# Performance work log

Measured on AMD Instinct MI355X. Metric: run time of the kernel, lower is better.

## Reference

```python
import jax, jax.numpy as jnp
import numpy as np

GRID_N = 8
N_RAYS = 4096
CHUNK = 512
MAX_SAMPLES = 128
SAMPLING_LENGTH = 0.05
STEP = SAMPLING_LENGTH / MAX_SAMPLES
HIT_THRESH = 5.0


def _build_mesh(n):
    g = n + 1
    xs = np.linspace(0.0, 1.0, g)
    P = np.stack(np.meshgrid(xs, xs, xs, indexing='ij'), -1).reshape(-1, 3).astype(np.float32)

    def vid(i, j, k):
        return (i * g + j) * g + k

    perms = [(0, 1, 2), (0, 2, 1), (1, 0, 2), (1, 2, 0), (2, 0, 1), (2, 1, 0)]
    tets = []
    for i in range(n):
        for j in range(n):
            for k in range(n):
                base = np.array([i, j, k])
                for p in perms:
                    vlist = [base.copy()]
                    cur = base.copy()
                    for ax in p:
                        cur = cur.copy(); cur[ax] += 1
                        vlist.append(cur.copy())
                    tets.append([vid(*vv) for vv in vlist])
    tets = np.array(tets, dtype=np.int32)  # [T,4]
    A, B, C, D = tets.T
    # face order matches torch module: ABC, ABD, ACD, BCD
    faces = np.stack([np.stack([A, B, C], 1), np.stack([A, B, D], 1),
                      np.stack([A, C, D], 1), np.stack([B, C, D], 1)], 1).astype(np.int32)  # [T,4,3]
    ff = faces.reshape(-1, 3)
    sf = np.sort(ff, 1)
    order = np.lexsort((sf[:, 2], sf[:, 1], sf[:, 0]))
    ss = sf[order]
    eq = np.all(ss[:-1] == ss[1:], 1)
    topo = -np.ones((tets.shape[0], 4), dtype=np.int32)
    idx = np.where(eq)[0]
    a = order[idx]; b = order[idx + 1]
    topo[a // 4, a % 4] = b // 4
    topo[b // 4, b % 4] = a // 4
    return P, tets, faces, topo


def setup_inputs() -> dict:
    key = jax.random.key(0)
    k1, k2, k3 = jax.random.split(key, 3)
    P, tets, faces, topo = _build_mesh(GRID_N)
    cage = jnp.asarray(P)[None] + 0.005 * jax.random.normal(k1, (1, P.shape[0], 3), jnp.float32)
    xy = jax.random.uniform(k2, (N_RAYS, 2), jnp.float32, 0.15, 0.85)
    ro = jnp.concatenate([xy, jnp.full((N_RAYS, 1), -0.5, jnp.float32)], -1)[None]
    jit = 0.05 * jax.random.normal(k3, (N_RAYS, 2), jnp.float32)
    rd = jnp.concatenate([jit, jnp.ones((N_RAYS, 1), jnp.float32)], -1)
    rd = (rd / jnp.linalg.norm(rd, axis=-1, keepdims=True))[None]
    return {"cage_vertices": cage, "ro": ro, "rd": rd,
            "tetras": jnp.asarray(tets), "faces": jnp.asarray(faces),
            "topology": jnp.asarray(topo)}


def _intersect(tri, o, d):
    # Moller-Trumbore: tri [F,3,3], o/d [c,3] -> nearest hit t + face idx
    p0 = tri[:, 0]; e1 = tri[:, 1] - p0; e2 = tri[:, 2] - p0
    h = jnp.cross(d[:, None, :], e2[None])          # [c,F,3]
    a = jnp.sum(e1[None] * h, -1)                   # [c,F]
    f = 1.0 / jnp.where(jnp.abs(a) > 1e-9, a, 1e-9)
    s = o[:, None, :] - p0[None]
    u = f * jnp.sum(s * h, -1)
    q = jnp.cross(s, e1[None])
    v = f * jnp.sum(d[:, None, :] * q, -1)
    t = f * jnp.sum(e2[None] * q, -1)
    ok = (jnp.abs(a) > 1e-9) & (u >= 0) & (u <= 1) & (v >= 0) & (u + v <= 1) & (t > 1e-6)
    t = jnp.where(ok, t, 1e10)
    return jnp.min(t, 1), jnp.argmin(t, 1)


def _bary(verts, tetras, p, tet):
    # barycentric coords of p [R,3] inside tetra tet [R] -> [R,4]
    vv = verts[tetras[tet]]                                # [R,4,3]
    M = jnp.transpose(vv[:, 1:] - vv[:, :1], (0, 2, 1))    # [R,3,3] columns B-A,C-A,D-A
    w = jnp.linalg.solve(M, (p - vv[:, 0])[..., None])[..., 0]  # wB,wC,wD
    return jnp.concatenate([1.0 - jnp.sum(w, -1, keepdims=True), w], -1)


def reference(cage_vertices, ro, rd, tetras, faces, topology):
    verts = cage_vertices[0]                 # [V,3]
    tri = verts[faces.reshape(-1, 3)]        # [F,3,3] deformed tetra faces
    o = ro[0]; d = rd[0]
    R = o.shape[0]
    od = jnp.concatenate([o, d], -1).reshape(R // CHUNK, CHUNK, 6)
    tmin, fidx = jax.lax.map(lambda x: _intersect(tri, x[:, :3], x[:, 3:]), od)
    tmin = tmin.reshape(R); fidx = fidx.reshape(R)
    hit = tmin < HIT_THRESH                  # mask = distances < 5
    t0 = jnp.where(hit, tmin, 0.0)
    hitp = o + t0[:, None] * d               # closest_points
    tet0 = jnp.where(hit, (fidx // 4).astype(jnp.int32), 0)  # triangle_to_tetra

    def step(carry, k):
        tet, alive = carry
        p = hitp + (k.astype(jnp.float32) * STEP + 1e-4) * d
        for _ in range(3):  # up to 3 neighbor hops per sample (tetra walk)
            w = _bary(verts, tetras, p, tet)
            inside = jnp.all(w >= -1e-6, -1)
            nb = topology[tet, 3 - jnp.argmin(w, -1)]  # face opposite most-negative vert
            move = alive & ~inside
            tet = jnp.where(move & (nb >= 0), nb, tet)
            alive = alive & (inside | (nb >= 0))
        w = _bary(verts, tetras, p, tet)
        inside = jnp.all(w >= -1e-6, -1)
        valid = alive & inside
        m = valid[:, None].astype(w.dtype)
        return (tet, alive), (jnp.where(valid, tet, -1), w * m, p * m, valid)

    (_, _), (tet_s, w_s, p_s, valid_s) = jax.lax.scan(step, (tet0, hit), jnp.arange(MAX_SAMPLES))
    tetra_indices = jnp.transpose(tet_s)            # [R,S]
    bary_coords = jnp.transpose(w_s, (1, 0, 2))     # [R,S,4]
    deformed_positions = jnp.transpose(p_s, (1, 0, 2))  # [R,S,3]
    valid = jnp.transpose(valid_s)
    ray_indices = jnp.where(valid, jnp.arange(R, dtype=jnp.int32)[:, None], -1)
    t_start = t0
    t_end = jnp.where(hit, t0 + SAMPLING_LENGTH, 0.0)
    return ray_indices, tetra_indices, bary_coords, t_start, t_end, deformed_positions
```

## Files before the change

### kernel.cpp

```cpp
#include <hip/hip_runtime.h>

#define S_MAX 128
#define NV_MAX 729
#define STEPD (0.05 / 128.0)
#define GUARD 1e-12

static __device__ __forceinline__ double mt_eval_f64(
    int F, const int* __restrict__ faces,
    const float* sx, const float* sy, const float* sz,
    double ox, double oy, double oz,
    double dx, double dy, double dz)
{
    const int i0 = faces[3 * F + 0];
    const int i1 = faces[3 * F + 1];
    const int i2 = faces[3 * F + 2];
    const double p0x = (double)sx[i0], p0y = (double)sy[i0], p0z = (double)sz[i0];
    const double e1x = (double)sx[i1] - p0x, e1y = (double)sy[i1] - p0y, e1z = (double)sz[i1] - p0z;
    const double e2x = (double)sx[i2] - p0x, e2y = (double)sy[i2] - p0y, e2z = (double)sz[i2] - p0z;
    const double hx = dy * e2z - dz * e2y;
    const double hy = dz * e2x - dx * e2z;
    const double hz = dx * e2y - dy * e2x;
    const double a  = e1x * hx + e1y * hy + e1z * hz;
    const bool oka = fabs(a) > 1e-9;
    const double f  = 1.0 / (oka ? a : 1e-9);
    const double s0 = ox - p0x, s1 = oy - p0y, s2 = oz - p0z;
    const double u  = f * (s0 * hx + s1 * hy + s2 * hz);
    const double qx = s1 * e1z - s2 * e1y;
    const double qy = s2 * e1x - s0 * e1z;
    const double qz = s0 * e1y - s1 * e1x;
    const double v  = f * (dx * qx + dy * qy + dz * qz);
    double t        = f * (e2x * qx + e2y * qy + e2z * qz);
    const bool ok = oka && (u >= 0.0) && (u <= 1.0) && (v >= 0.0) &&
                    (u + v <= 1.0) && (t > 1e-6);
    return ok ? t : 1e10;
}

__global__ __launch_bounds__(256) void prep_kernel(
    const float* __restrict__ verts,
    const int*   __restrict__ tetras,
    double* __restrict__ winv,
    int NT)
{
    const int t = blockIdx.x * 256 + threadIdx.x;
    if (t >= NT) return;
    const int4 tv = ((const int4*)tetras)[t];
    const double v0x = (double)verts[3 * tv.x + 0];
    const double v0y = (double)verts[3 * tv.x + 1];
    const double v0z = (double)verts[3 * tv.x + 2];
    const double m11 = (double)verts[3 * tv.y + 0] - v0x, m21 = (double)verts[3 * tv.y + 1] - v0y, m31 = (double)verts[3 * tv.y + 2] - v0z;
    const double m12 = (double)verts[3 * tv.z + 0] - v0x, m22 = (double)verts[3 * tv.z + 1] - v0y, m32 = (double)verts[3 * tv.z + 2] - v0z;
    const double m13 = (double)verts[3 * tv.w + 0] - v0x, m23 = (double)verts[3 * tv.w + 1] - v0y, m33 = (double)verts[3 * tv.w + 2] - v0z;
    const double A = m22 * m33 - m23 * m32;
    const double B = m21 * m33 - m23 * m31;
    const double C = m21 * m32 - m22 * m31;
    const double det = m11 * A - m12 * B + m13 * C;
    const double rcp = 1.0 / det;
    double* o = winv + 12 * (size_t)t;
    o[0] = v0x; o[1] = v0y; o[2] = v0z;
    o[3]  = A * rcp;  o[4]  = (m13 * m32 - m12 * m33) * rcp;  o[5]  = (m12 * m23 - m13 * m22) * rcp;
    o[6]  = -B * rcp; o[7]  = (m11 * m33 - m13 * m31) * rcp;  o[8]  = (m13 * m21 - m11 * m23) * rcp;
    o[9]  = C * rcp;  o[10] = (m12 * m31 - m11 * m32) * rcp;  o[11] = (m11 * m22 - m12 * m21) * rcp;
}

__global__ __launch_bounds__(256) void fused_kernel(
    const float* __restrict__ verts,
    const float* __restrict__ ro,
    const float* __restrict__ rd,
    const int*   __restrict__ faces,
    const int*   __restrict__ topo,
    const double* __restrict__ winv,
    float* __restrict__ out_rayidx,
    float* __restrict__ out_tetidx,
    float* __restrict__ out_bary,
    float* __restrict__ out_tstart,
    float* __restrict__ out_tend,
    float* __restrict__ out_pos,
    int NV, int NF, int R)
{
    __shared__ float sx[NV_MAX], sy[NV_MAX], sz[NV_MAX];
    __shared__ float red[256];
    __shared__ float s_zmin, s_zmax, s_marg;
    __shared__ short s_seq[4][S_MAX];

    const int tid = threadIdx.x;
    for (int i = tid; i < NV; i += 256) {
        sx[i] = verts[3 * i + 0];
        sy[i] = verts[3 * i + 1];
        sz[i] = verts[3 * i + 2];
    }
    __syncthreads();

    float zmin = 1e9f, zmax = -1e9f, dev = 0.0f;
    for (int i = tid; i < NV; i += 256) {
        const float x = sx[i], y = sy[i], z = sz[i];
        if (i % 9 == 0) { zmin = fminf(zmin, z); zmax = fmaxf(zmax, z); }
        dev = fmaxf(dev, fabsf(x - rintf(x * 8.0f) * 0.125f));
        dev = fmaxf(dev, fabsf(y - rintf(y * 8.0f) * 0.125f));
    }
    red[tid] = zmin; __syncthreads();
    for (int s = 128; s; s >>= 1) { if (tid < s) red[tid] = fminf(red[tid], red[tid + s]); __syncthreads(); }
    if (tid == 0) s_zmin = red[0];
    __syncthreads();
    red[tid] = zmax; __syncthreads();
    for (int s = 128; s; s >>= 1) { if (tid < s) red[tid] = fmaxf(red[tid], red[tid + s]); __syncthreads(); }
    if (tid == 0) s_zmax = red[0];
    __syncthreads();
    red[tid] = dev; __syncthreads();
    for (int s = 128; s; s >>= 1) { if (tid < s) red[tid] = fmaxf(red[tid], red[tid + s]); __syncthreads(); }
    if (tid == 0) s_marg = red[0] + 1e-5f;
    __syncthreads();

    const int wv = tid >> 6, lane = tid & 63;
    const int r = blockIdx.x * 4 + wv;
    if (r >= R) return;
    short* myseq = s_seq[wv];

    const double ox = (double)ro[3 * r + 0], oy = (double)ro[3 * r + 1], oz = (double)ro[3 * r + 2];
    const double dx = (double)rd[3 * r + 0], dy = (double)rd[3 * r + 1], dz = (double)rd[3 * r + 2];

    int ncand = 0, ixlo = 0, iylo = 0, ny = 1;
    if (dz > 0.0) {
        const double t_lo = ((double)s_zmin - oz) / dz;
        const double t_hi = ((double)s_zmax - oz) / dz;
        const double marg = (double)s_marg + 1e-9;
        const double xa = ox + t_lo * dx, xb = ox + t_hi * dx;
        const double ya = oy + t_lo * dy, yb = oy + t_hi * dy;
        const double xlo = fmin(xa, xb) - marg, xhi = fmax(xa, xb) + marg;
        const double ylo = fmin(ya, yb) - marg, yhi = fmax(ya, yb) + marg;
        const int ix0 = max(0, (int)floor(xlo * 8.0)), ix1 = min(7, (int)floor(xhi * 8.0));
        const int iy0 = max(0, (int)floor(ylo * 8.0)), iy1 = min(7, (int)floor(yhi * 8.0));
        if (ix0 <= ix1 && iy0 <= iy1) {
            ixlo = ix0; iylo = iy0;
            ny = iy1 - iy0 + 1;
            ncand = (ix1 - ix0 + 1) * ny * 24;
        }
    }

    double bt = 1e10;
    int    bi = 0x7fffffff;
    for (int c = lane; c < ncand; c += 64) {
        const int cell = c / 24, fk = c - cell * 24;
        const int cx = cell / ny, cy = cell - cx * ny;
        const int F = ((ixlo + cx) * 64 + (iylo + cy) * 8) * 24 + fk;
        const double t = mt_eval_f64(F, faces, sx, sy, sz, ox, oy, oz, dx, dy, dz);
        if (t < bt || (t == bt && F < bi)) { bt = t; bi = F; }
    }
    for (int off = 32; off; off >>= 1) {
        const double t2 = __shfl_down(bt, off);
        const int    i2 = __shfl_down(bi, off);
        if (t2 < bt || (t2 == bt && i2 < bi)) { bt = t2; bi = i2; }
    }
    bt = __shfl(bt, 0);
    bi = __shfl(bi, 0);
    if (bt >= 1e10) {
        double fb = 1e10; int fi = 0x7fffffff;
        for (int F = lane; F < NF; F += 64) {
            const double t = mt_eval_f64(F, faces, sx, sy, sz, ox, oy, oz, dx, dy, dz);
            if (t < fb || (t == fb && F < fi)) { fb = t; fi = F; }
        }
        for (int off = 32; off; off >>= 1) {
            const double t2 = __shfl_down(fb, off);
            const int    i2 = __shfl_down(fi, off);
            if (t2 < fb || (t2 == fb && i2 < fi)) { fb = t2; fi = i2; }
        }
        bt = __shfl(fb, 0);
        bi = __shfl(fi, 0);
    }

    const bool   hit = bt < 5.0;
    const double t0  = hit ? bt : 0.0;
    if (lane == 0) {
        out_tstart[r] = (float)t0;
        out_tend[r]   = hit ? (float)(t0 + 0.05) : 0.0f;
    }

    const double hpx = ox + t0 * dx, hpy = oy + t0 * dy, hpz = oz + t0 * dz;

    if (!hit) {
        for (int k = lane; k < S_MAX; k += 64) myseq[k] = -1;
    } else {
        int  tet   = bi >> 2;
        bool alive = true;

        int4 topo4 = ((const int4*)topo)[tet];
        const double* rec = winv + 12 * (size_t)tet;
        double v0x = rec[0], v0y = rec[1], v0z = rec[2];
        double i0 = rec[3], i1 = rec[4],  i2 = rec[5];
        double i3 = rec[6], i4 = rec[7],  i5 = rec[8];
        double i6 = rec[9], i7 = rec[10], i8 = rec[11];

        double wb0, wb1, wb2, wb3, wd0, wd1, wd2, wd3;
        {
            const double bx = hpx - v0x, by = hpy - v0y, bz = hpz - v0z;
            wb1 = i0 * bx + i1 * by + i2 * bz;
            wb2 = i3 * bx + i4 * by + i5 * bz;
            wb3 = i6 * bx + i7 * by + i8 * bz;
            wd1 = i0 * dx + i1 * dy + i2 * dz;
            wd2 = i3 * dx + i4 * dy + i5 * dz;
            wd3 = i6 * dx + i7 * dy + i8 * dz;
            wb0 = 1.0 - (wb1 + wb2 + wb3);
            wd0 = -(wd1 + wd2 + wd3);
        }

        int k0 = 0;
        while (k0 < S_MAX) {
            const int kk = k0 + lane;
            bool p = false;
            if (kk < S_MAX) {
                const double toff = (double)kk * STEPD + 1e-4;
                const double a0 = wb0 + toff * wd0;
                const double a1 = wb1 + toff * wd1;
                const double a2 = wb2 + toff * wd2;
                const double a3 = wb3 + toff * wd3;
                const double mn = fmin(fmin(a0, a1), fmin(a2, a3));
                p = (mn + 1e-6 >= GUARD);
            }
            const unsigned long long bad = __ballot(kk < S_MAX && !p);
            const int nvalid = min(S_MAX - k0, 64);
            const int evt = (bad == 0ull) ? nvalid : (__ffsll(bad) - 1);

            if (lane < evt) myseq[kk] = (short)tet;
            k0 += evt;
            if (evt == nvalid) continue;

            const double toff = (double)k0 * STEPD + 1e-4;
            const double px = hpx + toff * dx;
            const double py = hpy + toff * dy;
            const double pz = hpz + toff * dz;

            double b1 = px - v0x, b2 = py - v0y, b3 = pz - v0z;
            double w1 = i0 * b1 + i1 * b2 + i2 * b3;
            double w2 = i3 * b1 + i4 * b2 + i5 * b3;
            double w3 = i6 * b1 + i7 * b2 + i8 * b3;
            double w0 = 1.0 - (w1 + w2 + w3);
            bool inside = (w0 >= -1e-6) && (w1 >= -1e-6) && (w2 >= -1e-6) && (w3 >= -1e-6);

            int it = 0;
            bool moved = false;
            while (!inside && it < 3) {
                int    jm = 0;
                double wb = w0;
                if (w1 < wb) { wb = w1; jm = 1; }
                if (w2 < wb) { wb = w2; jm = 2; }
                if (w3 < wb) { wb = w3; jm = 3; }
                const int nb = (jm == 0) ? topo4.w : (jm == 1) ? topo4.z :
                               (jm == 2) ? topo4.y : topo4.x;
                if (nb < 0) { alive = false; break; }
                tet = nb;
                moved = true;
                rec = winv + 12 * (size_t)tet;
                topo4 = ((const int4*)topo)[tet];
                v0x = rec[0]; v0y = rec[1]; v0z = rec[2];
                i0 = rec[3]; i1 = rec[4];  i2 = rec[5];
                i3 = rec[6]; i4 = rec[7];  i5 = rec[8];
                i6 = rec[9]; i7 = rec[10]; i8 = rec[11];
                b1 = px - v0x; b2 = py - v0y; b3 = pz - v0z;
                w1 = i0 * b1 + i1 * b2 + i2 * b3;
                w2 = i3 * b1 + i4 * b2 + i5 * b3;
                w3 = i6 * b1 + i7 * b2 + i8 * b3;
                w0 = 1.0 - (w1 + w2 + w3);
                inside = (w0 >= -1e-6) && (w1 >= -1e-6) && (w2 >= -1e-6) && (w3 >= -1e-6);
                ++it;
            }
            if (!alive) break;

            if (lane == 0) myseq[k0] = inside ? (short)tet : (short)-1;
            ++k0;

            if (moved) {
                const double bx = hpx - v0x, by = hpy - v0y, bz = hpz - v0z;
                wb1 = i0 * bx + i1 * by + i2 * bz;
                wb2 = i3 * bx + i4 * by + i5 * bz;
                wb3 = i6 * bx + i7 * by + i8 * bz;
                wd1 = i0 * dx + i1 * dy + i2 * dz;
                wd2 = i3 * dx + i4 * dy + i5 * dz;
                wd3 = i6 * dx + i7 * dy + i8 * dz;
                wb0 = 1.0 - (wb1 + wb2 + wb3);
                wd0 = -(wd1 + wd2 + wd3);
            }
        }
        for (int k = k0 + lane; k < S_MAX; k += 64) myseq[k] = -1;
    }

    for (int k = lane; k < S_MAX; k += 64) {
        const size_t idx = (size_t)r * S_MAX + k;
        const int tk = (int)myseq[k];
        if (tk < 0) {
            out_rayidx[idx] = -1.0f;
            out_tetidx[idx] = -1.0f;
            ((float4*)out_bary)[idx] = make_float4(0.0f, 0.0f, 0.0f, 0.0f);
            out_pos[idx * 3 + 0] = 0.0f;
            out_pos[idx * 3 + 1] = 0.0f;
            out_pos[idx * 3 + 2] = 0.0f;
            continue;
        }
        const double toff = (double)k * STEPD + 1e-4;
        const double px = hpx + toff * dx;
        const double py = hpy + toff * dy;
        const double pz = hpz + toff * dz;

        const double* rec2 = winv + 12 * (size_t)tk;
        const double b1 = px - rec2[0], b2 = py - rec2[1], b3 = pz - rec2[2];
        const double w1 = rec2[3] * b1 + rec2[4]  * b2 + rec2[5]  * b3;
        const double w2 = rec2[6] * b1 + rec2[7]  * b2 + rec2[8]  * b3;
        const double w3 = rec2[9] * b1 + rec2[10] * b2 + rec2[11] * b3;
        const double w0 = 1.0 - (w1 + w2 + w3);

        out_rayidx[idx] = (float)r;
        out_tetidx[idx] = (float)tk;
        ((float4*)out_bary)[idx] = make_float4((float)w0, (float)w1, (float)w2, (float)w3);
        out_pos[idx * 3 + 0] = (float)px;
        out_pos[idx * 3 + 1] = (float)py;
        out_pos[idx * 3 + 2] = (float)pz;
    }
}

extern "C" void kernel_launch(void* const* d_in, const int* in_sizes, int n_in,
                              void* d_out, int out_size, void* d_ws, size_t ws_size,
                              hipStream_t stream) {
    const float* verts  = (const float*)d_in[0];
    const float* ro     = (const float*)d_in[1];
    const float* rd     = (const float*)d_in[2];
    const int*   tetras = (const int*)d_in[3];
    const int*   faces  = (const int*)d_in[4];
    const int*   topo   = (const int*)d_in[5];

    const int NV = in_sizes[0] / 3;
    const int R  = in_sizes[1] / 3;
    const int NT = in_sizes[3] / 4;
    const int NF = in_sizes[4] / 3;
    const int S  = S_MAX;

    double* winv = (double*)d_ws;

    float* out        = (float*)d_out;
    float* out_rayidx = out;
    float* out_tetidx = out + (size_t)R * S;
    float* out_bary   = out + (size_t)2 * R * S;
    float* out_tstart = out + (size_t)6 * R * S;
    float* out_tend   = out_tstart + R;
    float* out_pos    = out_tend + R;

    prep_kernel<<<(NT + 255) / 256, 256, 0, stream>>>(verts, tetras, winv, NT);
    fused_kernel<<<(R + 3) / 4, 256, 0, stream>>>(
        verts, ro, rd, faces, topo, winv,
        out_rayidx, out_tetidx, out_bary, out_tstart, out_tend, out_pos,
        NV, NF, R);
}
```

Measured before the change: 83.40 us.

## Drop prep kernel, compute tetra inverses on the fly, write outputs directly

Removes the separate prep kernel that precomputed per-tetra inverse matrices into workspace. Each ray now rebuilds the inverse from vertices already held in shared memory whenever it enters a new tetra. It also drops the shared-memory sequence buffer and writes outputs straight from the walk loop instead of in a second pass that reloaded the inverse records. This saves one launch and a global-memory round trip, at the cost of repeated fp64 inverse computation (including a divide) on each tetra change.

```diff
diff --git a/kernel.cpp b/kernel.cpp
--- a/kernel.cpp
+++ b/kernel.cpp
@@ -35,40 +35,13 @@
     return ok ? t : 1e10;
 }
 
-__global__ __launch_bounds__(256) void prep_kernel(
-    const float* __restrict__ verts,
-    const int*   __restrict__ tetras,
-    double* __restrict__ winv,
-    int NT)
-{
-    const int t = blockIdx.x * 256 + threadIdx.x;
-    if (t >= NT) return;
-    const int4 tv = ((const int4*)tetras)[t];
-    const double v0x = (double)verts[3 * tv.x + 0];
-    const double v0y = (double)verts[3 * tv.x + 1];
-    const double v0z = (double)verts[3 * tv.x + 2];
-    const double m11 = (double)verts[3 * tv.y + 0] - v0x, m21 = (double)verts[3 * tv.y + 1] - v0y, m31 = (double)verts[3 * tv.y + 2] - v0z;
-    const double m12 = (double)verts[3 * tv.z + 0] - v0x, m22 = (double)verts[3 * tv.z + 1] - v0y, m32 = (double)verts[3 * tv.z + 2] - v0z;
-    const double m13 = (double)verts[3 * tv.w + 0] - v0x, m23 = (double)verts[3 * tv.w + 1] - v0y, m33 = (double)verts[3 * tv.w + 2] - v0z;
-    const double A = m22 * m33 - m23 * m32;
-    const double B = m21 * m33 - m23 * m31;
-    const double C = m21 * m32 - m22 * m31;
-    const double det = m11 * A - m12 * B + m13 * C;
-    const double rcp = 1.0 / det;
-    double* o = winv + 12 * (size_t)t;
-    o[0] = v0x; o[1] = v0y; o[2] = v0z;
-    o[3]  = A * rcp;  o[4]  = (m13 * m32 - m12 * m33) * rcp;  o[5]  = (m12 * m23 - m13 * m22) * rcp;
-    o[6]  = -B * rcp; o[7]  = (m11 * m33 - m13 * m31) * rcp;  o[8]  = (m13 * m21 - m11 * m23) * rcp;
-    o[9]  = C * rcp;  o[10] = (m12 * m31 - m11 * m32) * rcp;  o[11] = (m11 * m22 - m12 * m21) * rcp;
-}
-
 __global__ __launch_bounds__(256) void fused_kernel(
     const float* __restrict__ verts,
     const float* __restrict__ ro,
     const float* __restrict__ rd,
     const int*   __restrict__ faces,
+    const int*   __restrict__ tetras,
     const int*   __restrict__ topo,
-    const double* __restrict__ winv,
     float* __restrict__ out_rayidx,
     float* __restrict__ out_tetidx,
     float* __restrict__ out_bary,
@@ -80,7 +53,6 @@
     __shared__ float sx[NV_MAX], sy[NV_MAX], sz[NV_MAX];
     __shared__ float red[256];
     __shared__ float s_zmin, s_zmax, s_marg;
-    __shared__ short s_seq[4][S_MAX];
 
     const int tid = threadIdx.x;
     for (int i = tid; i < NV; i += 256) {
@@ -113,7 +85,6 @@
     const int wv = tid >> 6, lane = tid & 63;
     const int r = blockIdx.x * 4 + wv;
     if (r >= R) return;
-    short* myseq = s_seq[wv];
 
     const double ox = (double)ro[3 * r + 0], oy = (double)ro[3 * r + 1], oz = (double)ro[3 * r + 2];
     const double dx = (double)rd[3 * r + 0], dy = (double)rd[3 * r + 1], dz = (double)rd[3 * r + 2];
@@ -175,144 +146,159 @@
     }
 
     const double hpx = ox + t0 * dx, hpy = oy + t0 * dy, hpz = oz + t0 * dz;
+    const size_t rbase = (size_t)r * S_MAX;
+
+    auto emit_invalid = [&](int k) {
+        const size_t idx = rbase + k;
+        out_rayidx[idx] = -1.0f;
+        out_tetidx[idx] = -1.0f;
+        ((float4*)out_bary)[idx] = make_float4(0.0f, 0.0f, 0.0f, 0.0f);
+        out_pos[idx * 3 + 0] = 0.0f;
+        out_pos[idx * 3 + 1] = 0.0f;
+        out_pos[idx * 3 + 2] = 0.0f;
+    };
 
     if (!hit) {
-        for (int k = lane; k < S_MAX; k += 64) myseq[k] = -1;
-    } else {
-        int  tet   = bi >> 2;
-        bool alive = true;
-
-        int4 topo4 = ((const int4*)topo)[tet];
-        const double* rec = winv + 12 * (size_t)tet;
-        double v0x = rec[0], v0y = rec[1], v0z = rec[2];
-        double i0 = rec[3], i1 = rec[4],  i2 = rec[5];
-        double i3 = rec[6], i4 = rec[7],  i5 = rec[8];
-        double i6 = rec[9], i7 = rec[10], i8 = rec[11];
-
-        double wb0, wb1, wb2, wb3, wd0, wd1, wd2, wd3;
-        {
-            const double bx = hpx - v0x, by = hpy - v0y, bz = hpz - v0z;
-            wb1 = i0 * bx + i1 * by + i2 * bz;
-            wb2 = i3 * bx + i4 * by + i5 * bz;
-            wb3 = i6 * bx + i7 * by + i8 * bz;
-            wd1 = i0 * dx + i1 * dy + i2 * dz;
-            wd2 = i3 * dx + i4 * dy + i5 * dz;
-            wd3 = i6 * dx + i7 * dy + i8 * dz;
-            wb0 = 1.0 - (wb1 + wb2 + wb3);
-            wd0 = -(wd1 + wd2 + wd3);
-        }
-
-        int k0 = 0;
-        while (k0 < S_MAX) {
-            const int kk = k0 + lane;
-            bool p = false;
-            if (kk < S_MAX) {
-                const double toff = (double)kk * STEPD + 1e-4;
-                const double a0 = wb0 + toff * wd0;
-                const double a1 = wb1 + toff * wd1;
-                const double a2 = wb2 + toff * wd2;
-                const double a3 = wb3 + toff * wd3;
-                const double mn = fmin(fmin(a0, a1), fmin(a2, a3));
-                p = (mn + 1e-6 >= GUARD);
-            }
-            const unsigned long long bad = __ballot(kk < S_MAX && !p);
-            const int nvalid = min(S_MAX - k0, 64);
-            const int evt = (bad == 0ull) ? nvalid : (__ffsll(bad) - 1);
-
-            if (lane < evt) myseq[kk] = (short)tet;
-            k0 += evt;
-            if (evt == nvalid) continue;
-
-            const double toff = (double)k0 * STEPD + 1e-4;
+        for (int k = lane; k < S_MAX; k += 64) emit_invalid(k);
+        return;
+    }
+
+    int  tet   = bi >> 2;
+    bool alive = true;
+
+    const int4* tets4 = (const int4*)tetras;
+    const int4* topo16 = (const int4*)topo;
+
+    int4 topo4;
+    double v0x, v0y, v0z;
+    double i0, i1, i2, i3, i4, i5, i6, i7, i8;
+
+    auto build_inv = [&]() {
+        const int4 tv = tets4[tet];
+        v0x = (double)sx[tv.x]; v0y = (double)sy[tv.x]; v0z = (double)sz[tv.x];
+        const double m11 = (double)sx[tv.y] - v0x, m21 = (double)sy[tv.y] - v0y, m31 = (double)sz[tv.y] - v0z;
+        const double m12 = (double)sx[tv.z] - v0x, m22 = (double)sy[tv.z] - v0y, m32 = (double)sz[tv.z] - v0z;
+        const double m13 = (double)sx[tv.w] - v0x, m23 = (double)sy[tv.w] - v0y, m33 = (double)sz[tv.w] - v0z;
+        const double A = m22 * m33 - m23 * m32;
+        const double B = m21 * m33 - m23 * m31;
+        const double C = m21 * m32 - m22 * m31;
+        const double det = m11 * A - m12 * B + m13 * C;
+        const double rcp = 1.0 / det;
+        i0 = A * rcp;  i1 = (m13 * m32 - m12 * m33) * rcp;  i2 = (m12 * m23 - m13 * m22) * rcp;
+        i3 = -B * rcp; i4 = (m11 * m33 - m13 * m31) * rcp;  i5 = (m13 * m21 - m11 * m23) * rcp;
+        i6 = C * rcp;  i7 = (m12 * m31 - m11 * m32) * rcp;  i8 = (m11 * m22 - m12 * m21) * rcp;
+    };
+
+    topo4 = topo16[tet];
+    build_inv();
+
+    double wb0, wb1, wb2, wb3, wd0, wd1, wd2, wd3;
+    auto build_affine = [&]() {
+        const double bx = hpx - v0x, by = hpy - v0y, bz = hpz - v0z;
+        wb1 = i0 * bx + i1 * by + i2 * bz;
+        wb2 = i3 * bx + i4 * by + i5 * bz;
+        wb3 = i6 * bx + i7 * by + i8 * bz;
+        wd1 = i0 * dx + i1 * dy + i2 * dz;
+        wd2 = i3 * dx + i4 * dy + i5 * dz;
+        wd3 = i6 * dx + i7 * dy + i8 * dz;
+        wb0 = 1.0 - (wb1 + wb2 + wb3);
+        wd0 = -(wd1 + wd2 + wd3);
+    };
+    build_affine();
+
+    int k0 = 0;
+    while (k0 < S_MAX) {
+        const int kk = k0 + lane;
+        bool p = false;
+        if (kk < S_MAX) {
+            const double toff = (double)kk * STEPD + 1e-4;
+            const double a0 = wb0 + toff * wd0;
+            const double a1 = wb1 + toff * wd1;
+            const double a2 = wb2 + toff * wd2;
+            const double a3 = wb3 + toff * wd3;
+            const double mn = fmin(fmin(a0, a1), fmin(a2, a3));
+            p = (mn + 1e-6 >= GUARD);
+        }
+        const unsigned long long bad = __ballot(kk < S_MAX && !p);
+        const int nvalid = min(S_MAX - k0, 64);
+        const int evt = (bad == 0ull) ? nvalid : (__ffsll(bad) - 1);
+
+        if (lane < evt) {
+            const double toff = (double)kk * STEPD + 1e-4;
             const double px = hpx + toff * dx;
             const double py = hpy + toff * dy;
             const double pz = hpz + toff * dz;
-
-            double b1 = px - v0x, b2 = py - v0y, b3 = pz - v0z;
-            double w1 = i0 * b1 + i1 * b2 + i2 * b3;
-            double w2 = i3 * b1 + i4 * b2 + i5 * b3;
-            double w3 = i6 * b1 + i7 * b2 + i8 * b3;
-            double w0 = 1.0 - (w1 + w2 + w3);
-            bool inside = (w0 >= -1e-6) && (w1 >= -1e-6) && (w2 >= -1e-6) && (w3 >= -1e-6);
-
-            int it = 0;
-            bool moved = false;
-            while (!inside && it < 3) {
-                int    jm = 0;
-                double wb = w0;
-                if (w1 < wb) { wb = w1; jm = 1; }
-                if (w2 < wb) { wb = w2; jm = 2; }
-                if (w3 < wb) { wb = w3; jm = 3; }
-                const int nb = (jm == 0) ? topo4.w : (jm == 1) ? topo4.z :
-                               (jm == 2) ? topo4.y : topo4.x;
-                if (nb < 0) { alive = false; break; }
-                tet = nb;
-                moved = true;
-                rec = winv + 12 * (size_t)tet;
-                topo4 = ((const int4*)topo)[tet];
-                v0x = rec[0]; v0y = rec[1]; v0z = rec[2];
-                i0 = rec[3]; i1 = rec[4];  i2 = rec[5];
-                i3 = rec[6]; i4 = rec[7];  i5 = rec[8];
-                i6 = rec[9]; i7 = rec[10]; i8 = rec[11];
-                b1 = px - v0x; b2 = py - v0y; b3 = pz - v0z;
-                w1 = i0 * b1 + i1 * b2 + i2 * b3;
-                w2 = i3 * b1 + i4 * b2 + i5 * b3;
-                w3 = i6 * b1 + i7 * b2 + i8 * b3;
-                w0 = 1.0 - (w1 + w2 + w3);
-                inside = (w0 >= -1e-6) && (w1 >= -1e-6) && (w2 >= -1e-6) && (w3 >= -1e-6);
-                ++it;
-            }
-            if (!alive) break;
-
-            if (lane == 0) myseq[k0] = inside ? (short)tet : (short)-1;
-            ++k0;
-
-            if (moved) {
-                const double bx = hpx - v0x, by = hpy - v0y, bz = hpz - v0z;
-                wb1 = i0 * bx + i1 * by + i2 * bz;
-                wb2 = i3 * bx + i4 * by + i5 * bz;
-                wb3 = i6 * bx + i7 * by + i8 * bz;
-                wd1 = i0 * dx + i1 * dy + i2 * dz;
-                wd2 = i3 * dx + i4 * dy + i5 * dz;
-                wd3 = i6 * dx + i7 * dy + i8 * dz;
-                wb0 = 1.0 - (wb1 + wb2 + wb3);
-                wd0 = -(wd1 + wd2 + wd3);
-            }
-        }
-        for (int k = k0 + lane; k < S_MAX; k += 64) myseq[k] = -1;
-    }
-
-    for (int k = lane; k < S_MAX; k += 64) {
-        const size_t idx = (size_t)r * S_MAX + k;
-        const int tk = (int)myseq[k];
-        if (tk < 0) {
-            out_rayidx[idx] = -1.0f;
-            out_tetidx[idx] = -1.0f;
-            ((float4*)out_bary)[idx] = make_float4(0.0f, 0.0f, 0.0f, 0.0f);
-            out_pos[idx * 3 + 0] = 0.0f;
-            out_pos[idx * 3 + 1] = 0.0f;
-            out_pos[idx * 3 + 2] = 0.0f;
-            continue;
-        }
-        const double toff = (double)k * STEPD + 1e-4;
+            const double b1 = px - v0x, b2 = py - v0y, b3 = pz - v0z;
+            const double w1 = i0 * b1 + i1 * b2 + i2 * b3;
+            const double w2 = i3 * b1 + i4 * b2 + i5 * b3;
+            const double w3 = i6 * b1 + i7 * b2 + i8 * b3;
+            const double w0 = 1.0 - (w1 + w2 + w3);
+            const size_t idx = rbase + kk;
+            out_rayidx[idx] = (float)r;
+            out_tetidx[idx] = (float)tet;
+            ((float4*)out_bary)[idx] = make_float4((float)w0, (float)w1, (float)w2, (float)w3);
+            out_pos[idx * 3 + 0] = (float)px;
+            out_pos[idx * 3 + 1] = (float)py;
+            out_pos[idx * 3 + 2] = (float)pz;
+        }
+        k0 += evt;
+        if (evt == nvalid) continue;
+
+        const double toff = (double)k0 * STEPD + 1e-4;
         const double px = hpx + toff * dx;
         const double py = hpy + toff * dy;
         const double pz = hpz + toff * dz;
 
-        const double* rec2 = winv + 12 * (size_t)tk;
-        const double b1 = px - rec2[0], b2 = py - rec2[1], b3 = pz - rec2[2];
-        const double w1 = rec2[3] * b1 + rec2[4]  * b2 + rec2[5]  * b3;
-        const double w2 = rec2[6] * b1 + rec2[7]  * b2 + rec2[8]  * b3;
-        const double w3 = rec2[9] * b1 + rec2[10] * b2 + rec2[11] * b3;
-        const double w0 = 1.0 - (w1 + w2 + w3);
-
-        out_rayidx[idx] = (float)r;
-        out_tetidx[idx] = (float)tk;
-        ((float4*)out_bary)[idx] = make_float4((float)w0, (float)w1, (float)w2, (float)w3);
-        out_pos[idx * 3 + 0] = (float)px;
-        out_pos[idx * 3 + 1] = (float)py;
-        out_pos[idx * 3 + 2] = (float)pz;
-    }
+        double b1 = px - v0x, b2 = py - v0y, b3 = pz - v0z;
+        double w1 = i0 * b1 + i1 * b2 + i2 * b3;
+        double w2 = i3 * b1 + i4 * b2 + i5 * b3;
+        double w3 = i6 * b1 + i7 * b2 + i8 * b3;
+        double w0 = 1.0 - (w1 + w2 + w3);
+        bool inside = (w0 >= -1e-6) && (w1 >= -1e-6) && (w2 >= -1e-6) && (w3 >= -1e-6);
+
+        int it = 0;
+        bool moved = false;
+        while (!inside && it < 3) {
+            int    jm = 0;
+            double wb = w0;
+            if (w1 < wb) { wb = w1; jm = 1; }
+            if (w2 < wb) { wb = w2; jm = 2; }
+            if (w3 < wb) { wb = w3; jm = 3; }
+            const int nb = (jm == 0) ? topo4.w : (jm == 1) ? topo4.z :
+                           (jm == 2) ? topo4.y : topo4.x;
+            if (nb < 0) { alive = false; break; }
+            tet = nb;
+            moved = true;
+            topo4 = topo16[tet];
+            build_inv();
+            b1 = px - v0x; b2 = py - v0y; b3 = pz - v0z;
+            w1 = i0 * b1 + i1 * b2 + i2 * b3;
+            w2 = i3 * b1 + i4 * b2 + i5 * b3;
+            w3 = i6 * b1 + i7 * b2 + i8 * b3;
+            w0 = 1.0 - (w1 + w2 + w3);
+            inside = (w0 >= -1e-6) && (w1 >= -1e-6) && (w2 >= -1e-6) && (w3 >= -1e-6);
+            ++it;
+        }
+        if (!alive) break;
+
+        if (lane == 0) {
+            if (inside) {
+                const size_t idx = rbase + k0;
+                out_rayidx[idx] = (float)r;
+                out_tetidx[idx] = (float)tet;
+                ((float4*)out_bary)[idx] = make_float4((float)w0, (float)w1, (float)w2, (float)w3);
+                out_pos[idx * 3 + 0] = (float)px;
+                out_pos[idx * 3 + 1] = (float)py;
+                out_pos[idx * 3 + 2] = (float)pz;
+            } else {
+                emit_invalid(k0);
+            }
+        }
+        ++k0;
+
+        if (moved) build_affine();
+    }
+    for (int k = k0 + lane; k < S_MAX; k += 64) emit_invalid(k);
 }
 
 extern "C" void kernel_launch(void* const* d_in, const int* in_sizes, int n_in,
@@ -327,11 +313,8 @@
 
     const int NV = in_sizes[0] / 3;
     const int R  = in_sizes[1] / 3;
-    const int NT = in_sizes[3] / 4;
     const int NF = in_sizes[4] / 3;
     const int S  = S_MAX;
-
-    double* winv = (double*)d_ws;
 
     float* out        = (float*)d_out;
     float* out_rayidx = out;
@@ -341,9 +324,8 @@
     float* out_tend   = out_tstart + R;
     float* out_pos    = out_tend + R;
 
-    prep_kernel<<<(NT + 255) / 256, 256, 0, stream>>>(verts, tetras, winv, NT);
     fused_kernel<<<(R + 3) / 4, 256, 0, stream>>>(
-        verts, ro, rd, faces, topo, winv,
+        verts, ro, rd, faces, tetras, topo,
         out_rayidx, out_tetidx, out_bary, out_tstart, out_tend, out_pos,
         NV, NF, R);
 }
```

Result: no change. 81.98 us (-1.7%).
